# Optimization experiments

Measured on AMD Instinct MI355X. Metric: run time of the kernel, lower is better.

Reference implementation:

```python
import jax, jax.numpy as jnp
import numpy as np

DIM = 128
HEADS = 4
WS = 8  # window size
HEAD_DIM = DIM // HEADS
LOG100 = float(np.log(100.0))


def _cpb_constants(ws):
    # log-spaced relative coordinates table, shape [(2ws-1)^2, 2]
    rng = np.arange(-(ws - 1), ws, dtype=np.float32)
    table = np.stack(np.meshgrid(rng, rng, indexing='ij'), axis=-1)  # [2ws-1,2ws-1,2]
    table = table / (ws - 1)
    table = table * 8.0
    table = np.sign(table) * np.log2(np.abs(table) + 1.0) / np.log2(8.0)
    table = table.reshape(-1, 2)
    # relative position index, shape [ws^2, ws^2]
    coords = np.stack(np.meshgrid(np.arange(ws), np.arange(ws), indexing='ij'), axis=0).reshape(2, -1)
    rel = coords[:, :, None] - coords[:, None, :]  # [2, ws^2, ws^2]
    idx = (rel[0] + ws - 1) * (2 * ws - 1) + (rel[1] + ws - 1)
    return jnp.asarray(table), jnp.asarray(idx.astype(np.int32))


def setup_inputs() -> dict:
    key = jax.random.key(0)
    ks = jax.random.split(key, 10)
    B, H, W = 16, 128, 128
    nW = (H // WS) * (W // WS)
    return {
        'x': jax.random.normal(ks[0], (B, H, W, DIM), jnp.float32),
        'mask': jnp.zeros((nW, WS * WS, WS * WS), jnp.float32),
        'qkv_w': jax.random.normal(ks[1], (DIM, 3 * DIM), jnp.float32) * 0.02,
        'q_bias': jax.random.normal(ks[2], (DIM,), jnp.float32) * 0.02,
        'v_bias': jax.random.normal(ks[3], (DIM,), jnp.float32) * 0.02,
        'logit_scale': jnp.full((HEADS,), float(np.log(10.0)), jnp.float32),
        'cpb_w1': jax.random.normal(ks[4], (2, 512), jnp.float32) * 0.02,
        'cpb_b1': jax.random.normal(ks[5], (512,), jnp.float32) * 0.02,
        'cpb_w2': jax.random.normal(ks[6], (512, HEADS), jnp.float32) * 0.02,
        'proj_w': jax.random.normal(ks[7], (DIM, DIM), jnp.float32) * 0.02,
        'proj_b': jax.random.normal(ks[8], (DIM,), jnp.float32) * 0.02,
        'height': 128,
        'width': 128,
    }


def reference(x, mask, qkv_w, q_bias, v_bias, logit_scale, cpb_w1, cpb_b1, cpb_w2, proj_w, proj_b, height, width):
    B = x.shape[0]
    N = WS * WS
    wh, ww = height // WS, width // WS
    nW = wh * ww

    # QKV projection, K has no bias
    qkv_b = jnp.concatenate([q_bias, jnp.zeros_like(q_bias), v_bias])
    qkv = x @ qkv_w + qkv_b  # [B,H,W,3*DIM]

    # fused window partition -> [3, B*nW, heads, N, head_dim]
    qkv = qkv.reshape(B, wh, WS, ww, WS, 3, HEADS, HEAD_DIM)
    qkv = jnp.transpose(qkv, (5, 0, 1, 3, 6, 2, 4, 7)).reshape(3, B * nW, HEADS, N, HEAD_DIM)
    q, k, v = qkv[0], qkv[1], qkv[2]

    # cosine attention with clamped learnable temperature
    q = q / jnp.maximum(jnp.linalg.norm(q, axis=-1, keepdims=True), 1e-12)
    k = k / jnp.maximum(jnp.linalg.norm(k, axis=-1, keepdims=True), 1e-12)
    scale = jnp.exp(jnp.minimum(logit_scale, LOG100))  # [heads]
    attn = jnp.einsum('whqd,whkd->whqk', q, k) * scale[None, :, None, None]

    # continuous relative position bias via small MLP
    table, idx = _cpb_constants(WS)
    bias_tab = jax.nn.relu(table @ cpb_w1 + cpb_b1) @ cpb_w2  # [(2ws-1)^2, heads]
    bias = 16.0 * jax.nn.sigmoid(bias_tab[idx])  # [N, N, heads]
    attn = attn + jnp.transpose(bias, (2, 0, 1))[None]

    # shifted-window mask
    attn = attn.reshape(B, nW, HEADS, N, N) + mask[None, :, None, :, :]
    attn = jax.nn.softmax(attn.reshape(B * nW, HEADS, N, N), axis=-1)

    out = jnp.einsum('whqk,whkd->whqd', attn, v)  # [B*nW, heads, N, head_dim]

    # fused window reverse -> [B, H, W, DIM]
    out = out.reshape(B, wh, ww, HEADS, WS, WS, HEAD_DIM)
    out = jnp.transpose(out, (0, 1, 4, 2, 5, 3, 6)).reshape(B, height, width, DIM)

    return out @ proj_w + proj_b
```

## Files before the change

kernel.cpp:

```cpp
#include <hip/hip_runtime.h>

typedef unsigned short u16;
typedef __bf16 bf16x8 __attribute__((ext_vector_type(8)));
typedef float f32x4 __attribute__((ext_vector_type(4)));
typedef int i32x4 __attribute__((ext_vector_type(4)));
typedef int i32x2 __attribute__((ext_vector_type(2)));
typedef i32x4 i32x4_a __attribute__((may_alias));
typedef i32x2 i32x2_a __attribute__((may_alias));
typedef bf16x8 bf16x8_a __attribute__((may_alias));
typedef f32x4 f32x4_a __attribute__((may_alias));
typedef unsigned long long u64_a __attribute__((may_alias));

__device__ __forceinline__ float bf2f(u16 u) {
  union { unsigned int i; float f; } c;
  c.i = ((unsigned int)u) << 16;
  return c.f;
}
__device__ __forceinline__ u16 f2bf(float f) {
  union { __bf16 h; u16 u; } c;
  c.h = (__bf16)f;
  return c.u;
}
__device__ __forceinline__ float gld(const void* p, int i, int isbf) {
  return isbf ? bf2f(((const u16*)p)[i]) : ((const float*)p)[i];
}
__device__ __forceinline__ int sw(int row, int col, int rs) {
  return row * rs + ((((col >> 3) ^ (row & 7)) << 3) | (col & 7));
}

#define WQKVT_OFF 0
#define PWT_OFF   98304
#define QKVB_OFF  131072
#define BIAS_OFF  132608
#define SCALE_OFF 198144
#define PB_OFF    198160
#define FLAG_OFF  198672
#define MASKF_OFF 200704
#define MASKF_NEED (200704ull + 4ull * 1024 * 1024)

__global__ void swin_detect(const unsigned int* __restrict__ xw,
                            unsigned int* __restrict__ flag) {
  int t = threadIdx.x;
  int cnt = 0;
  for (int i = 0; i < 8; i++) {
    unsigned int w = xw[t * 8 + i];
    unsigned int lo = w & 0xffffu;
    unsigned int e = (lo >> 7) & 0xffu;
    if ((e >= 0x70u && e <= 0x82u) || lo == 0u) cnt++;
  }
  cnt += __shfl_xor(cnt, 1);
  cnt += __shfl_xor(cnt, 2);
  cnt += __shfl_xor(cnt, 4);
  cnt += __shfl_xor(cnt, 8);
  cnt += __shfl_xor(cnt, 16);
  cnt += __shfl_xor(cnt, 32);
  if (t == 0) *flag = (cnt >= 256) ? 1u : 0u;
}

__global__ void swin_setup(const void* __restrict__ qkv_w, const void* __restrict__ q_bias,
                           const void* __restrict__ v_bias, const void* __restrict__ ls,
                           const void* __restrict__ cpb_w1, const void* __restrict__ cpb_b1,
                           const void* __restrict__ cpb_w2, const void* __restrict__ proj_w,
                           const void* __restrict__ proj_b, char* __restrict__ ws) {
  const int b = blockIdx.x, t = threadIdx.x;
  const int isbf = (int)*(const unsigned int*)(ws + FLAG_OFF);
  u16* wqkvF = (u16*)(ws + WQKVT_OFF);
  u16* pwF = (u16*)(ws + PWT_OFF);
  float* qkvb = (float*)(ws + QKVB_OFF);
  float* bias16F = (float*)(ws + BIAS_OFF);
  float* scalef = (float*)(ws + SCALE_OFF);
  float* pbf = (float*)(ws + PB_OFF);

  if (b < 128) {
    int ks = b >> 5, lq = (b >> 3) & 3, j = b & 7;
    for (int c = t; c < 384; c += 256) {
      int sub = c / 96, rr = c % 96;
      int nt = rr >> 4, l16 = rr & 15;
      int addr = (((sub * 6 + nt) * 4 + ks) << 9) + ((lq * 16 + l16) << 3) + j;
      wqkvF[addr] = f2bf(gld(qkv_w, b * 384 + c, isbf));
    }
  } else if (b < 256) {
    int r = b - 128;
    int ks = r >> 5, lq = (r >> 3) & 3, j = r & 7;
    if (t < 128) {
      int sub = t >> 5, rr = t & 31;
      int nt = rr >> 4, l16 = rr & 15;
      int addr = (((sub * 2 + nt) * 4 + ks) << 9) + ((lq * 16 + l16) << 3) + j;
      pwF[addr] = f2bf(gld(proj_w, r * 128 + t, isbf));
    }
  } else if (b == 256) {
    for (int o = t; o < 384; o += 256) {
      float v = 0.f;
      if (o < 128) v = gld(q_bias, o, isbf);
      else if (o >= 256) v = gld(v_bias, o - 256, isbf);
      qkvb[o] = v;
    }
    if (t < 128) pbf[t] = gld(proj_b, t, isbf);
    if (t < 4) scalef[t] = expf(fminf(gld(ls, t, isbf), 4.60517019f));
  } else {
    __shared__ float w1[1024];
    __shared__ float b1[512];
    __shared__ float w2[2048];
    __shared__ float tab[225][4];
    for (int i = t; i < 1024; i += 256) w1[i] = gld(cpb_w1, i, isbf);
    for (int i = t; i < 512; i += 256) b1[i] = gld(cpb_b1, i, isbf);
    for (int i = t; i < 2048; i += 256) w2[i] = gld(cpb_w2, i, isbf);
    __syncthreads();
    if (t < 225) {
      int i = t / 15, j = t % 15;
      float c0, c1;
      {
        float tt = ((float)(i - 7) / 7.0f) * 8.0f;
        float s = (tt > 0.f) ? 1.f : ((tt < 0.f) ? -1.f : 0.f);
        c0 = s * log2f(fabsf(tt) + 1.f) / 3.0f;
      }
      {
        float tt = ((float)(j - 7) / 7.0f) * 8.0f;
        float s = (tt > 0.f) ? 1.f : ((tt < 0.f) ? -1.f : 0.f);
        c1 = s * log2f(fabsf(tt) + 1.f) / 3.0f;
      }
      float acc[4] = {0.f, 0.f, 0.f, 0.f};
      for (int jj = 0; jj < 512; jj++) {
        float h = fmaxf(c0 * w1[jj] + c1 * w1[512 + jj] + b1[jj], 0.f);
        #pragma unroll
        for (int hh = 0; hh < 4; hh++) acc[hh] += h * w2[jj * 4 + hh];
      }
      #pragma unroll
      for (int hh = 0; hh < 4; hh++) tab[t][hh] = acc[hh];
    }
    __syncthreads();
    for (int e = t; e < 4 * 64 * 64; e += 256) {
      int h = e >> 12, mg = (e >> 11) & 1, qt = (e >> 10) & 1;
      int kt = (e >> 8) & 3, lane = (e >> 2) & 63, r = e & 3;
      int q = 32 * mg + 16 * qt + (lane & 15);
      int kk = 16 * kt + 4 * (lane >> 4) + r;
      int dr = (q >> 3) - (kk >> 3) + 7;
      int dc = (q & 7) - (kk & 7) + 7;
      float v = tab[dr * 15 + dc][h];
      bias16F[e] = 16.f / (1.f + expf(-v));
    }
  }
}

__global__ void swin_setup_mask(const void* __restrict__ mask, char* __restrict__ ws) {
  const int w = blockIdx.x, t = threadIdx.x;
  const int isbf = (int)*(const unsigned int*)(ws + FLAG_OFF);
  float* maskF = (float*)(ws + MASKF_OFF);
  #pragma unroll
  for (int i = 0; i < 16; i++) {
    int e = t + i * 256;
    int q = e >> 6, k = e & 63;
    int mg = q >> 5, qt = (q >> 4) & 1, l16 = q & 15;
    int kt = k >> 4, lq = (k >> 2) & 3, r = k & 3;
    int addr = w * 4096 + ((mg * 2 + qt) * 4 + kt) * 256 + ((lq * 16 + l16) << 2) + r;
    maskF[addr] = gld(mask, w * 4096 + e, isbf);
  }
}

#define X_OFF 0
#define Q_OFF 8192
#define K_OFF 16384
#define VT_OFF 24576
#define P_OFF 0
#define AO_OFF 16384

template <int MF>
__global__ __launch_bounds__(512, 4) void swin_main(
    const void* __restrict__ x, const void* __restrict__ mask,
    const char* __restrict__ ws, void* __restrict__ out) {
  __shared__ __align__(16) u16 lds[32768];
  const f32x4 fz = {0.f, 0.f, 0.f, 0.f};

  const u16* wqkvF = (const u16*)(ws + WQKVT_OFF);
  const u16* pwF = (const u16*)(ws + PWT_OFF);
  const float* qkvb = (const float*)(ws + QKVB_OFF);
  const float* bias16F = (const float*)(ws + BIAS_OFF);
  const float* scalef = (const float*)(ws + SCALE_OFF);
  const float* pbf = (const float*)(ws + PB_OFF);
  const int isbf = (int)*(const unsigned int*)(ws + FLAG_OFF);

  const int tid = threadIdx.x;
  const int wid = tid >> 6;
  const int lane = tid & 63;
  const int ln16 = lane & 15;
  const int lq = lane >> 4;
  const int q8 = lq << 3;
  const int mg = wid >> 2;
  const int sub = wid & 3;

  const int wi = blockIdx.x;
  const int b = wi >> 8;
  const int rem = wi & 255;
  const int wy = rem >> 4, wx = rem & 15;
  const int xbase = ((b * 128 + wy * 8) * 128 + wx * 8) * 128;

  if (isbf) {
    const u16* xb = (const u16*)x;
    #pragma unroll
    for (int rep = 0; rep < 2; rep++) {
      int ch = tid + rep * 512;
      int token = ch >> 4, dch = ch & 15;
      int r = token >> 3, c = token & 7;
      i32x4 v = *(const i32x4_a*)(xb + xbase + r * 16384 + c * 128 + dch * 8);
      *(i32x4_a*)(lds + X_OFF + sw(token, dch * 8, 128)) = v;
    }
  } else {
    const float* xf = (const float*)x;
    #pragma unroll
    for (int rep = 0; rep < 2; rep++) {
      int ch = tid + rep * 512;
      int token = ch >> 4, dch = ch & 15;
      int r = token >> 3, c = token & 7;
      const float* src = xf + xbase + r * 16384 + c * 128 + dch * 8;
      union { i32x4 v2[2]; float f[8]; } in;
      in.v2[0] = *(const i32x4_a*)(src);
      in.v2[1] = *(const i32x4_a*)(src + 4);
      union { u16 u[8]; i32x4 v; } o;
      #pragma unroll
      for (int d = 0; d < 8; d++) o.u[d] = f2bf(in.f[d]);
      *(i32x4_a*)(lds + X_OFF + sw(token, dch * 8, 128)) = o.v;
    }
  }
  __syncthreads();

  f32x4 acc1[2][6];
  #pragma unroll
  for (int nt = 0; nt < 6; nt++) {
    float bv = qkvb[96 * sub + 16 * nt + ln16];
    f32x4 ci = {bv, bv, bv, bv};
    acc1[0][nt] = ci;
    acc1[1][nt] = ci;
  }

  #pragma unroll
  for (int ks = 0; ks < 4; ks++) {
    bf16x8 a0 = *(const bf16x8_a*)(lds + X_OFF + sw(32 * mg + ln16, 32 * ks + q8, 128));
    bf16x8 a1 = *(const bf16x8_a*)(lds + X_OFF + sw(32 * mg + 16 + ln16, 32 * ks + q8, 128));
    bf16x8 bb[6];
    #pragma unroll
    for (int nt = 0; nt < 6; nt++)
      bb[nt] = *(const bf16x8_a*)(wqkvF + (((sub * 6 + nt) * 4 + ks) << 9) + lane * 8);
    #pragma unroll
    for (int nt = 0; nt < 6; nt++) {
      acc1[0][nt] = __builtin_amdgcn_mfma_f32_16x16x32_bf16(a0, bb[nt], acc1[0][nt], 0, 0, 0);
      acc1[1][nt] = __builtin_amdgcn_mfma_f32_16x16x32_bf16(a1, bb[nt], acc1[1][nt], 0, 0, 0);
    }
  }

  #pragma unroll
  for (int ci = 0; ci < 3; ci++) {
    int n0 = 96 * sub + 32 * ci;
    int type = n0 >> 7;
    int head = (n0 & 127) >> 5;
    int nt0 = 2 * ci, nt1 = nt0 + 1;
    if (type < 2) {
      int base = (type == 0) ? Q_OFF : K_OFF;
      float sh = (type == 0) ? scalef[head] : 1.0f;
      #pragma unroll
      for (int mt = 0; mt < 2; mt++)
        #pragma unroll
        for (int r = 0; r < 4; r++) {
          float x0 = acc1[mt][nt0][r], x1 = acc1[mt][nt1][r];
          float ss = x0 * x0 + x1 * x1;
          ss += __shfl_xor(ss, 1);
          ss += __shfl_xor(ss, 2);
          ss += __shfl_xor(ss, 4);
          ss += __shfl_xor(ss, 8);
          float inv = sh / fmaxf(sqrtf(ss), 1e-12f);
          int row = 32 * mg + 16 * mt + 4 * lq + r;
          lds[base + sw(row, head * 32 + ln16, 128)] = f2bf(x0 * inv);
          lds[base + sw(row, head * 32 + 16 + ln16, 128)] = f2bf(x1 * inv);
        }
    } else {
      #pragma unroll
      for (int mt = 0; mt < 2; mt++) {
        int c0 = 32 * mg + 16 * mt + 4 * lq;
        unsigned int w0 = (unsigned int)f2bf(acc1[mt][nt0][0]) | ((unsigned int)f2bf(acc1[mt][nt0][1]) << 16);
        unsigned int w1 = (unsigned int)f2bf(acc1[mt][nt0][2]) | ((unsigned int)f2bf(acc1[mt][nt0][3]) << 16);
        i32x2 wv = {(int)w0, (int)w1};
        *(i32x2_a*)(lds + VT_OFF + sw(head * 32 + ln16, c0, 64)) = wv;
        unsigned int u0 = (unsigned int)f2bf(acc1[mt][nt1][0]) | ((unsigned int)f2bf(acc1[mt][nt1][1]) << 16);
        unsigned int u1 = (unsigned int)f2bf(acc1[mt][nt1][2]) | ((unsigned int)f2bf(acc1[mt][nt1][3]) << 16);
        i32x2 uv = {(int)u0, (int)u1};
        *(i32x2_a*)(lds + VT_OFF + sw(head * 32 + 16 + ln16, c0, 64)) = uv;
      }
    }
  }
  __syncthreads();

  const int h = sub;
  f32x4 ST[4][2];
  if (MF) {
    const float* mrow = (const float*)(ws + MASKF_OFF) + rem * 4096;
    #pragma unroll
    for (int qt = 0; qt < 2; qt++)
      #pragma unroll
      for (int kt = 0; kt < 4; kt++) {
        int fo = mg * 2048 + qt * 1024 + kt * 256 + lane * 4;
        f32x4 bv = *(const f32x4_a*)(bias16F + h * 4096 + fo);
        f32x4 mv = *(const f32x4_a*)(mrow + fo);
        ST[kt][qt] = bv + mv;
      }
  } else {
    const u16* mk16 = (const u16*)mask;
    const float* mkf = (const float*)mask;
    #pragma unroll
    for (int qt = 0; qt < 2; qt++) {
      int q = 32 * mg + 16 * qt + ln16;
      #pragma unroll
      for (int kt = 0; kt < 4; kt++) {
        f32x4 bv = *(const f32x4_a*)(bias16F + h * 4096 + mg * 2048 + qt * 1024 + kt * 256 + lane * 4);
        int bi = q * 64 + 16 * kt + 4 * lq;
        f32x4 cv;
        if (isbf) {
          u64_a mw = *(const u64_a*)(mk16 + rem * 4096 + bi);
          cv[0] = bv[0] + bf2f((u16)mw);
          cv[1] = bv[1] + bf2f((u16)(mw >> 16));
          cv[2] = bv[2] + bf2f((u16)(mw >> 32));
          cv[3] = bv[3] + bf2f((u16)(mw >> 48));
        } else {
          f32x4 mv = *(const f32x4_a*)(mkf + rem * 4096 + bi);
          cv = bv + mv;
        }
        ST[kt][qt] = cv;
      }
    }
  }

  bf16x8 kf[4], qf[2];
  #pragma unroll
  for (int kt = 0; kt < 4; kt++)
    kf[kt] = *(const bf16x8_a*)(lds + K_OFF + sw(16 * kt + ln16, h * 32 + q8, 128));
  #pragma unroll
  for (int qt = 0; qt < 2; qt++)
    qf[qt] = *(const bf16x8_a*)(lds + Q_OFF + sw(32 * mg + 16 * qt + ln16, h * 32 + q8, 128));

  #pragma unroll
  for (int kt = 0; kt < 4; kt++)
    #pragma unroll
    for (int qt = 0; qt < 2; qt++)
      ST[kt][qt] = __builtin_amdgcn_mfma_f32_16x16x32_bf16(kf[kt], qf[qt], ST[kt][qt], 0, 0, 0);

  #pragma unroll
  for (int qt = 0; qt < 2; qt++) {
    float m = ST[0][qt][0];
    #pragma unroll
    for (int kt = 0; kt < 4; kt++)
      #pragma unroll
      for (int r = 0; r < 4; r++) m = fmaxf(m, ST[kt][qt][r]);
    m = fmaxf(m, __shfl_xor(m, 16));
    m = fmaxf(m, __shfl_xor(m, 32));
    float sum = 0.f;
    #pragma unroll
    for (int kt = 0; kt < 4; kt++)
      #pragma unroll
      for (int r = 0; r < 4; r++) {
        float p = __expf(ST[kt][qt][r] - m);
        ST[kt][qt][r] = p;
        sum += p;
      }
    sum += __shfl_xor(sum, 16);
    sum += __shfl_xor(sum, 32);
    float inv = 1.0f / sum;
    #pragma unroll
    for (int kt = 0; kt < 4; kt++)
      #pragma unroll
      for (int r = 0; r < 4; r++) ST[kt][qt][r] *= inv;
  }
  __syncthreads();

  #pragma unroll
  for (int qt = 0; qt < 2; qt++)
    #pragma unroll
    for (int kt = 0; kt < 4; kt++) {
      int row = 32 * mg + 16 * qt + ln16;
      int col = h * 64 + 16 * kt + 4 * lq;
      unsigned int w0 = (unsigned int)f2bf(ST[kt][qt][0]) | ((unsigned int)f2bf(ST[kt][qt][1]) << 16);
      unsigned int w1 = (unsigned int)f2bf(ST[kt][qt][2]) | ((unsigned int)f2bf(ST[kt][qt][3]) << 16);
      i32x2 wv = {(int)w0, (int)w1};
      *(i32x2_a*)(lds + P_OFF + sw(row, col, 256)) = wv;
    }
  f32x4 O[2][2];
  O[0][0] = fz; O[0][1] = fz; O[1][0] = fz; O[1][1] = fz;
  #pragma unroll
  for (int ks = 0; ks < 2; ks++) {
    bf16x8 pf[2], vf[2];
    #pragma unroll
    for (int mt = 0; mt < 2; mt++)
      pf[mt] = *(const bf16x8_a*)(lds + P_OFF + sw(32 * mg + 16 * mt + ln16, h * 64 + 32 * ks + q8, 256));
    #pragma unroll
    for (int nt = 0; nt < 2; nt++)
      vf[nt] = *(const bf16x8_a*)(lds + VT_OFF + sw(h * 32 + 16 * nt + ln16, 32 * ks + q8, 64));
    #pragma unroll
    for (int mt = 0; mt < 2; mt++)
      #pragma unroll
      for (int nt = 0; nt < 2; nt++)
        O[mt][nt] = __builtin_amdgcn_mfma_f32_16x16x32_bf16(pf[mt], vf[nt], O[mt][nt], 0, 0, 0);
  }
  #pragma unroll
  for (int mt = 0; mt < 2; mt++)
    #pragma unroll
    for (int nt = 0; nt < 2; nt++)
      #pragma unroll
      for (int r = 0; r < 4; r++) {
        int row = 32 * mg + 16 * mt + 4 * lq + r;
        lds[AO_OFF + sw(row, h * 32 + 16 * nt + ln16, 128)] = f2bf(O[mt][nt][r]);
      }
  __syncthreads();

  float pb0 = pbf[32 * sub + ln16];
  float pb1 = pbf[32 * sub + 16 + ln16];
  f32x4 acc3[2][2];
  {
    f32x4 c0 = {pb0, pb0, pb0, pb0};
    f32x4 c1 = {pb1, pb1, pb1, pb1};
    acc3[0][0] = c0; acc3[0][1] = c1; acc3[1][0] = c0; acc3[1][1] = c1;
  }
  #pragma unroll
  for (int ks = 0; ks < 4; ks++) {
    bf16x8 a0 = *(const bf16x8_a*)(lds + AO_OFF + sw(32 * mg + ln16, 32 * ks + q8, 128));
    bf16x8 a1 = *(const bf16x8_a*)(lds + AO_OFF + sw(32 * mg + 16 + ln16, 32 * ks + q8, 128));
    bf16x8 b0 = *(const bf16x8_a*)(pwF + (((sub * 2 + 0) * 4 + ks) << 9) + lane * 8);
    bf16x8 b1 = *(const bf16x8_a*)(pwF + (((sub * 2 + 1) * 4 + ks) << 9) + lane * 8);
    acc3[0][0] = __builtin_amdgcn_mfma_f32_16x16x32_bf16(a0, b0, acc3[0][0], 0, 0, 0);
    acc3[0][1] = __builtin_amdgcn_mfma_f32_16x16x32_bf16(a0, b1, acc3[0][1], 0, 0, 0);
    acc3[1][0] = __builtin_amdgcn_mfma_f32_16x16x32_bf16(a1, b0, acc3[1][0], 0, 0, 0);
    acc3[1][1] = __builtin_amdgcn_mfma_f32_16x16x32_bf16(a1, b1, acc3[1][1], 0, 0, 0);
  }
  if (isbf) {
    u16* ob = (u16*)out;
    #pragma unroll
    for (int mt = 0; mt < 2; mt++)
      #pragma unroll
      for (int r = 0; r < 4; r++) {
        int row = 32 * mg + 16 * mt + 4 * lq + r;
        int o = xbase + (row >> 3) * 16384 + (row & 7) * 128 + 32 * sub;
        ob[o + ln16] = f2bf(acc3[mt][0][r]);
        ob[o + 16 + ln16] = f2bf(acc3[mt][1][r]);
      }
  } else {
    float* of = (float*)out;
    #pragma unroll
    for (int mt = 0; mt < 2; mt++)
      #pragma unroll
      for (int r = 0; r < 4; r++) {
        int row = 32 * mg + 16 * mt + 4 * lq + r;
        int o = xbase + (row >> 3) * 16384 + (row & 7) * 128 + 32 * sub;
        of[o + ln16] = acc3[mt][0][r];
        of[o + 16 + ln16] = acc3[mt][1][r];
      }
  }
}

extern "C" void kernel_launch(void* const* d_in, const int* in_sizes, int n_in,
                              void* d_out, int out_size, void* d_ws, size_t ws_size,
                              hipStream_t stream) {
  const void* x      = d_in[0];
  const void* mask   = d_in[1];
  const void* qkv_w  = d_in[2];
  const void* q_bias = d_in[3];
  const void* v_bias = d_in[4];
  const void* ls     = d_in[5];
  const void* cpb_w1 = d_in[6];
  const void* cpb_b1 = d_in[7];
  const void* cpb_w2 = d_in[8];
  const void* proj_w = d_in[9];
  const void* proj_b = d_in[10];
  const int B = in_sizes[0] / (128 * 128 * 128);

  char* ws = (char*)d_ws;
  swin_detect<<<1, 64, 0, stream>>>((const unsigned int*)x,
                                    (unsigned int*)(ws + FLAG_OFF));
  swin_setup<<<258, 256, 0, stream>>>(qkv_w, q_bias, v_bias, ls, cpb_w1, cpb_b1,
                                      cpb_w2, proj_w, proj_b, ws);
  if (ws_size >= MASKF_NEED) {
    swin_setup_mask<<<256, 256, 0, stream>>>(mask, ws);
    swin_main<1><<<B * 256, 512, 0, stream>>>(x, mask, ws, d_out);
  } else {
    swin_main<0><<<B * 256, 512, 0, stream>>>(x, mask, ws, d_out);
  }
}
```

Before: 363.5 us.

## Shrink LDS and registers by head-aligned QKV split, Q aliasing X, and exp2 softmax

Each wave now computes only its own head's 32 columns of K, V and Q in three sequential passes instead of a 96-column block at once. This cuts the accumulator register count, and Q is written over the X staging buffer so the LDS footprint drops from 64KB to 48KB. Together these allow launch bounds of 6 blocks per CU instead of 4. The softmax is moved to base 2 by folding log2e into the bias, mask and q scale and calling exp2f, and the norm uses rsqrt. In exchange, the A fragments of X are reloaded three times, and an extra barrier is added before the output is written into the region that aliases P.

```diff
diff --git a/kernel.cpp b/kernel.cpp
--- a/kernel.cpp
+++ b/kernel.cpp
@@ -11,6 +11,8 @@
 typedef f32x4 f32x4_a __attribute__((may_alias));
 typedef unsigned long long u64_a __attribute__((may_alias));
 
+#define LOG2E 1.4426950408889634f
+
 __device__ __forceinline__ float bf2f(u16 u) {
   union { unsigned int i; float f; } c;
   c.i = ((unsigned int)u) << 16;
@@ -26,6 +28,10 @@
 }
 __device__ __forceinline__ int sw(int row, int col, int rs) {
   return row * rs + ((((col >> 3) ^ (row & 7)) << 3) | (col & 7));
+}
+__device__ __forceinline__ f32x4 splat4(float x) {
+  f32x4 v = {x, x, x, x};
+  return v;
 }
 
 #define WQKVT_OFF 0
@@ -74,9 +80,8 @@
   if (b < 128) {
     int ks = b >> 5, lq = (b >> 3) & 3, j = b & 7;
     for (int c = t; c < 384; c += 256) {
-      int sub = c / 96, rr = c % 96;
-      int nt = rr >> 4, l16 = rr & 15;
-      int addr = (((sub * 6 + nt) * 4 + ks) << 9) + ((lq * 16 + l16) << 3) + j;
+      int ntg = c >> 4, l16 = c & 15;
+      int addr = ((ntg * 4 + ks) << 9) + ((lq * 16 + l16) << 3) + j;
       wqkvF[addr] = f2bf(gld(qkv_w, b * 384 + c, isbf));
     }
   } else if (b < 256) {
@@ -137,7 +142,7 @@
       int dr = (q >> 3) - (kk >> 3) + 7;
       int dc = (q & 7) - (kk & 7) + 7;
       float v = tab[dr * 15 + dc][h];
-      bias16F[e] = 16.f / (1.f + expf(-v));
+      bias16F[e] = LOG2E * (16.f / (1.f + expf(-v)));
     }
   }
 }
@@ -153,22 +158,21 @@
     int mg = q >> 5, qt = (q >> 4) & 1, l16 = q & 15;
     int kt = k >> 4, lq = (k >> 2) & 3, r = k & 3;
     int addr = w * 4096 + ((mg * 2 + qt) * 4 + kt) * 256 + ((lq * 16 + l16) << 2) + r;
-    maskF[addr] = gld(mask, w * 4096 + e, isbf);
-  }
-}
-
-#define X_OFF 0
-#define Q_OFF 8192
-#define K_OFF 16384
-#define VT_OFF 24576
+    maskF[addr] = LOG2E * gld(mask, w * 4096 + e, isbf);
+  }
+}
+
+#define XQ_OFF 0
+#define K_OFF 8192
+#define VT_OFF 16384
 #define P_OFF 0
 #define AO_OFF 16384
 
 template <int MF>
-__global__ __launch_bounds__(512, 4) void swin_main(
+__global__ __launch_bounds__(512, 6) void swin_main(
     const void* __restrict__ x, const void* __restrict__ mask,
     const char* __restrict__ ws, void* __restrict__ out) {
-  __shared__ __align__(16) u16 lds[32768];
+  __shared__ __align__(16) u16 lds[24576];
   const f32x4 fz = {0.f, 0.f, 0.f, 0.f};
 
   const u16* wqkvF = (const u16*)(ws + WQKVT_OFF);
@@ -202,7 +206,7 @@
       int token = ch >> 4, dch = ch & 15;
       int r = token >> 3, c = token & 7;
       i32x4 v = *(const i32x4_a*)(xb + xbase + r * 16384 + c * 128 + dch * 8);
-      *(i32x4_a*)(lds + X_OFF + sw(token, dch * 8, 128)) = v;
+      *(i32x4_a*)(lds + XQ_OFF + sw(token, dch * 8, 128)) = v;
     }
   } else {
     const float* xf = (const float*)x;
@@ -218,74 +222,127 @@
       union { u16 u[8]; i32x4 v; } o;
       #pragma unroll
       for (int d = 0; d < 8; d++) o.u[d] = f2bf(in.f[d]);
-      *(i32x4_a*)(lds + X_OFF + sw(token, dch * 8, 128)) = o.v;
+      *(i32x4_a*)(lds + XQ_OFF + sw(token, dch * 8, 128)) = o.v;
     }
   }
   __syncthreads();
 
-  f32x4 acc1[2][6];
-  #pragma unroll
-  for (int nt = 0; nt < 6; nt++) {
-    float bv = qkvb[96 * sub + 16 * nt + ln16];
-    f32x4 ci = {bv, bv, bv, bv};
-    acc1[0][nt] = ci;
-    acc1[1][nt] = ci;
-  }
-
-  #pragma unroll
-  for (int ks = 0; ks < 4; ks++) {
-    bf16x8 a0 = *(const bf16x8_a*)(lds + X_OFF + sw(32 * mg + ln16, 32 * ks + q8, 128));
-    bf16x8 a1 = *(const bf16x8_a*)(lds + X_OFF + sw(32 * mg + 16 + ln16, 32 * ks + q8, 128));
-    bf16x8 bb[6];
-    #pragma unroll
-    for (int nt = 0; nt < 6; nt++)
-      bb[nt] = *(const bf16x8_a*)(wqkvF + (((sub * 6 + nt) * 4 + ks) << 9) + lane * 8);
-    #pragma unroll
-    for (int nt = 0; nt < 6; nt++) {
-      acc1[0][nt] = __builtin_amdgcn_mfma_f32_16x16x32_bf16(a0, bb[nt], acc1[0][nt], 0, 0, 0);
-      acc1[1][nt] = __builtin_amdgcn_mfma_f32_16x16x32_bf16(a1, bb[nt], acc1[1][nt], 0, 0, 0);
-    }
-  }
-
-  #pragma unroll
-  for (int ci = 0; ci < 3; ci++) {
-    int n0 = 96 * sub + 32 * ci;
-    int type = n0 >> 7;
-    int head = (n0 & 127) >> 5;
-    int nt0 = 2 * ci, nt1 = nt0 + 1;
-    if (type < 2) {
-      int base = (type == 0) ? Q_OFF : K_OFF;
-      float sh = (type == 0) ? scalef[head] : 1.0f;
-      #pragma unroll
-      for (int mt = 0; mt < 2; mt++)
-        #pragma unroll
-        for (int r = 0; r < 4; r++) {
-          float x0 = acc1[mt][nt0][r], x1 = acc1[mt][nt1][r];
-          float ss = x0 * x0 + x1 * x1;
-          ss += __shfl_xor(ss, 1);
-          ss += __shfl_xor(ss, 2);
-          ss += __shfl_xor(ss, 4);
-          ss += __shfl_xor(ss, 8);
-          float inv = sh / fmaxf(sqrtf(ss), 1e-12f);
-          int row = 32 * mg + 16 * mt + 4 * lq + r;
-          lds[base + sw(row, head * 32 + ln16, 128)] = f2bf(x0 * inv);
-          lds[base + sw(row, head * 32 + 16 + ln16, 128)] = f2bf(x1 * inv);
-        }
-    } else {
-      #pragma unroll
-      for (int mt = 0; mt < 2; mt++) {
-        int c0 = 32 * mg + 16 * mt + 4 * lq;
-        unsigned int w0 = (unsigned int)f2bf(acc1[mt][nt0][0]) | ((unsigned int)f2bf(acc1[mt][nt0][1]) << 16);
-        unsigned int w1 = (unsigned int)f2bf(acc1[mt][nt0][2]) | ((unsigned int)f2bf(acc1[mt][nt0][3]) << 16);
-        i32x2 wv = {(int)w0, (int)w1};
-        *(i32x2_a*)(lds + VT_OFF + sw(head * 32 + ln16, c0, 64)) = wv;
-        unsigned int u0 = (unsigned int)f2bf(acc1[mt][nt1][0]) | ((unsigned int)f2bf(acc1[mt][nt1][1]) << 16);
-        unsigned int u1 = (unsigned int)f2bf(acc1[mt][nt1][2]) | ((unsigned int)f2bf(acc1[mt][nt1][3]) << 16);
-        i32x2 uv = {(int)u0, (int)u1};
-        *(i32x2_a*)(lds + VT_OFF + sw(head * 32 + 16 + ln16, c0, 64)) = uv;
-      }
-    }
-  }
+  const float sc_q = scalef[sub] * LOG2E;
+  f32x4 acc[2][2];
+  unsigned int hq[8];
+
+  {
+    const int n0 = 128 + 32 * sub;
+    const int ntg = n0 >> 4;
+    acc[0][0] = splat4(qkvb[n0 + ln16]);
+    acc[0][1] = splat4(qkvb[n0 + 16 + ln16]);
+    acc[1][0] = acc[0][0];
+    acc[1][1] = acc[0][1];
+    #pragma unroll
+    for (int ks = 0; ks < 4; ks++) {
+      bf16x8 a0 = *(const bf16x8_a*)(lds + XQ_OFF + sw(32 * mg + ln16, 32 * ks + q8, 128));
+      bf16x8 a1 = *(const bf16x8_a*)(lds + XQ_OFF + sw(32 * mg + 16 + ln16, 32 * ks + q8, 128));
+      bf16x8 b0 = *(const bf16x8_a*)(wqkvF + ((ntg * 4 + ks) << 9) + lane * 8);
+      bf16x8 b1 = *(const bf16x8_a*)(wqkvF + (((ntg + 1) * 4 + ks) << 9) + lane * 8);
+      acc[0][0] = __builtin_amdgcn_mfma_f32_16x16x32_bf16(a0, b0, acc[0][0], 0, 0, 0);
+      acc[0][1] = __builtin_amdgcn_mfma_f32_16x16x32_bf16(a0, b1, acc[0][1], 0, 0, 0);
+      acc[1][0] = __builtin_amdgcn_mfma_f32_16x16x32_bf16(a1, b0, acc[1][0], 0, 0, 0);
+      acc[1][1] = __builtin_amdgcn_mfma_f32_16x16x32_bf16(a1, b1, acc[1][1], 0, 0, 0);
+    }
+    #pragma unroll
+    for (int mt = 0; mt < 2; mt++)
+      #pragma unroll
+      for (int r = 0; r < 4; r++) {
+        float x0 = acc[mt][0][r], x1 = acc[mt][1][r];
+        float ss = x0 * x0 + x1 * x1;
+        ss += __shfl_xor(ss, 1);
+        ss += __shfl_xor(ss, 2);
+        ss += __shfl_xor(ss, 4);
+        ss += __shfl_xor(ss, 8);
+        float inv = rsqrtf(fmaxf(ss, 1e-24f));
+        int row = 32 * mg + 16 * mt + 4 * lq + r;
+        lds[K_OFF + sw(row, sub * 32 + ln16, 128)] = f2bf(x0 * inv);
+        lds[K_OFF + sw(row, sub * 32 + 16 + ln16, 128)] = f2bf(x1 * inv);
+      }
+  }
+  asm volatile("" ::: "memory");
+
+  {
+    const int n0 = 256 + 32 * sub;
+    const int ntg = n0 >> 4;
+    acc[0][0] = splat4(qkvb[n0 + ln16]);
+    acc[0][1] = splat4(qkvb[n0 + 16 + ln16]);
+    acc[1][0] = acc[0][0];
+    acc[1][1] = acc[0][1];
+    #pragma unroll
+    for (int ks = 0; ks < 4; ks++) {
+      bf16x8 a0 = *(const bf16x8_a*)(lds + XQ_OFF + sw(32 * mg + ln16, 32 * ks + q8, 128));
+      bf16x8 a1 = *(const bf16x8_a*)(lds + XQ_OFF + sw(32 * mg + 16 + ln16, 32 * ks + q8, 128));
+      bf16x8 b0 = *(const bf16x8_a*)(wqkvF + ((ntg * 4 + ks) << 9) + lane * 8);
+      bf16x8 b1 = *(const bf16x8_a*)(wqkvF + (((ntg + 1) * 4 + ks) << 9) + lane * 8);
+      acc[0][0] = __builtin_amdgcn_mfma_f32_16x16x32_bf16(a0, b0, acc[0][0], 0, 0, 0);
+      acc[0][1] = __builtin_amdgcn_mfma_f32_16x16x32_bf16(a0, b1, acc[0][1], 0, 0, 0);
+      acc[1][0] = __builtin_amdgcn_mfma_f32_16x16x32_bf16(a1, b0, acc[1][0], 0, 0, 0);
+      acc[1][1] = __builtin_amdgcn_mfma_f32_16x16x32_bf16(a1, b1, acc[1][1], 0, 0, 0);
+    }
+    #pragma unroll
+    for (int mt = 0; mt < 2; mt++) {
+      int c0 = 32 * mg + 16 * mt + 4 * lq;
+      unsigned int w0 = (unsigned int)f2bf(acc[mt][0][0]) | ((unsigned int)f2bf(acc[mt][0][1]) << 16);
+      unsigned int w1 = (unsigned int)f2bf(acc[mt][0][2]) | ((unsigned int)f2bf(acc[mt][0][3]) << 16);
+      i32x2 wv = {(int)w0, (int)w1};
+      *(i32x2_a*)(lds + VT_OFF + sw(sub * 32 + ln16, c0, 64)) = wv;
+      unsigned int u0 = (unsigned int)f2bf(acc[mt][1][0]) | ((unsigned int)f2bf(acc[mt][1][1]) << 16);
+      unsigned int u1 = (unsigned int)f2bf(acc[mt][1][2]) | ((unsigned int)f2bf(acc[mt][1][3]) << 16);
+      i32x2 uv = {(int)u0, (int)u1};
+      *(i32x2_a*)(lds + VT_OFF + sw(sub * 32 + 16 + ln16, c0, 64)) = uv;
+    }
+  }
+  asm volatile("" ::: "memory");
+
+  {
+    const int n0 = 32 * sub;
+    const int ntg = n0 >> 4;
+    acc[0][0] = splat4(qkvb[n0 + ln16]);
+    acc[0][1] = splat4(qkvb[n0 + 16 + ln16]);
+    acc[1][0] = acc[0][0];
+    acc[1][1] = acc[0][1];
+    #pragma unroll
+    for (int ks = 0; ks < 4; ks++) {
+      bf16x8 a0 = *(const bf16x8_a*)(lds + XQ_OFF + sw(32 * mg + ln16, 32 * ks + q8, 128));
+      bf16x8 a1 = *(const bf16x8_a*)(lds + XQ_OFF + sw(32 * mg + 16 + ln16, 32 * ks + q8, 128));
+      bf16x8 b0 = *(const bf16x8_a*)(wqkvF + ((ntg * 4 + ks) << 9) + lane * 8);
+      bf16x8 b1 = *(const bf16x8_a*)(wqkvF + (((ntg + 1) * 4 + ks) << 9) + lane * 8);
+      acc[0][0] = __builtin_amdgcn_mfma_f32_16x16x32_bf16(a0, b0, acc[0][0], 0, 0, 0);
+      acc[0][1] = __builtin_amdgcn_mfma_f32_16x16x32_bf16(a0, b1, acc[0][1], 0, 0, 0);
+      acc[1][0] = __builtin_amdgcn_mfma_f32_16x16x32_bf16(a1, b0, acc[1][0], 0, 0, 0);
+      acc[1][1] = __builtin_amdgcn_mfma_f32_16x16x32_bf16(a1, b1, acc[1][1], 0, 0, 0);
+    }
+    #pragma unroll
+    for (int mt = 0; mt < 2; mt++)
+      #pragma unroll
+      for (int r = 0; r < 4; r++) {
+        float x0 = acc[mt][0][r], x1 = acc[mt][1][r];
+        float ss = x0 * x0 + x1 * x1;
+        ss += __shfl_xor(ss, 1);
+        ss += __shfl_xor(ss, 2);
+        ss += __shfl_xor(ss, 4);
+        ss += __shfl_xor(ss, 8);
+        float inv = sc_q * rsqrtf(fmaxf(ss, 1e-24f));
+        hq[mt * 4 + r] = (unsigned int)f2bf(x0 * inv) | ((unsigned int)f2bf(x1 * inv) << 16);
+      }
+  }
+  __syncthreads();
+
+  #pragma unroll
+  for (int mt = 0; mt < 2; mt++)
+    #pragma unroll
+    for (int r = 0; r < 4; r++) {
+      unsigned int pv = hq[mt * 4 + r];
+      int row = 32 * mg + 16 * mt + 4 * lq + r;
+      lds[XQ_OFF + sw(row, sub * 32 + ln16, 128)] = (u16)(pv & 0xffffu);
+      lds[XQ_OFF + sw(row, sub * 32 + 16 + ln16, 128)] = (u16)(pv >> 16);
+    }
   __syncthreads();
 
   const int h = sub;
@@ -314,13 +371,13 @@
         f32x4 cv;
         if (isbf) {
           u64_a mw = *(const u64_a*)(mk16 + rem * 4096 + bi);
-          cv[0] = bv[0] + bf2f((u16)mw);
-          cv[1] = bv[1] + bf2f((u16)(mw >> 16));
-          cv[2] = bv[2] + bf2f((u16)(mw >> 32));
-          cv[3] = bv[3] + bf2f((u16)(mw >> 48));
+          cv[0] = bv[0] + bf2f((u16)mw) * LOG2E;
+          cv[1] = bv[1] + bf2f((u16)(mw >> 16)) * LOG2E;
+          cv[2] = bv[2] + bf2f((u16)(mw >> 32)) * LOG2E;
+          cv[3] = bv[3] + bf2f((u16)(mw >> 48)) * LOG2E;
         } else {
           f32x4 mv = *(const f32x4_a*)(mkf + rem * 4096 + bi);
-          cv = bv + mv;
+          cv = bv + mv * LOG2E;
         }
         ST[kt][qt] = cv;
       }
@@ -333,7 +390,7 @@
     kf[kt] = *(const bf16x8_a*)(lds + K_OFF + sw(16 * kt + ln16, h * 32 + q8, 128));
   #pragma unroll
   for (int qt = 0; qt < 2; qt++)
-    qf[qt] = *(const bf16x8_a*)(lds + Q_OFF + sw(32 * mg + 16 * qt + ln16, h * 32 + q8, 128));
+    qf[qt] = *(const bf16x8_a*)(lds + XQ_OFF + sw(32 * mg + 16 * qt + ln16, h * 32 + q8, 128));
 
   #pragma unroll
   for (int kt = 0; kt < 4; kt++)
@@ -355,7 +412,7 @@
     for (int kt = 0; kt < 4; kt++)
       #pragma unroll
       for (int r = 0; r < 4; r++) {
-        float p = __expf(ST[kt][qt][r] - m);
+        float p = exp2f(ST[kt][qt][r] - m);
         ST[kt][qt][r] = p;
         sum += p;
       }
@@ -397,6 +454,7 @@
       for (int nt = 0; nt < 2; nt++)
         O[mt][nt] = __builtin_amdgcn_mfma_f32_16x16x32_bf16(pf[mt], vf[nt], O[mt][nt], 0, 0, 0);
   }
+  __syncthreads();
   #pragma unroll
   for (int mt = 0; mt < 2; mt++)
     #pragma unroll
@@ -411,11 +469,8 @@
   float pb0 = pbf[32 * sub + ln16];
   float pb1 = pbf[32 * sub + 16 + ln16];
   f32x4 acc3[2][2];
-  {
-    f32x4 c0 = {pb0, pb0, pb0, pb0};
-    f32x4 c1 = {pb1, pb1, pb1, pb1};
-    acc3[0][0] = c0; acc3[0][1] = c1; acc3[1][0] = c0; acc3[1][1] = c1;
-  }
+  acc3[0][0] = splat4(pb0); acc3[0][1] = splat4(pb1);
+  acc3[1][0] = acc3[0][0];  acc3[1][1] = acc3[0][1];
   #pragma unroll
   for (int ks = 0; ks < 4; ks++) {
     bf16x8 a0 = *(const bf16x8_a*)(lds + AO_OFF + sw(32 * mg + ln16, 32 * ks + q8, 128));
```

After: 384.9 us. 5.9% more time.
